# Optimization experiments

Measured on AMD Instinct MI355X. Metric: run time of the kernel, lower is better.

Reference implementation:

```python
import jax, jax.numpy as jnp
import numpy as np
import math

B, N, T, CI, CO = 4, 2048, 64, 32, 32
K, TAU = 6, 3


def _cheb(x, gso, k_order):
    # x: [b,n,t,c] complex, gso: [n,n] complex -> [K,b,n,t,c]
    polys = [x]
    if k_order > 1:
        polys.append(jnp.einsum('nm,bmtc->bntc', gso, x))
    for _ in range(2, k_order):
        polys.append(2.0 * jnp.einsum('nm,bmtc->bntc', gso, polys[-1]) - polys[-2])
    return jnp.stack(polys)


def _lag(p, tau):
    # shift along time axis (-2) by tau, zero-padding at the front
    if tau == 0:
        return p
    pad = jnp.zeros_like(p[..., :tau, :])
    return jnp.concatenate([pad, p[..., :-tau, :]], axis=-2)


def setup_inputs() -> dict:
    key = jax.random.key(0)
    ks = jax.random.split(key, 6)
    scale = 1.0 / math.sqrt(K * TAU * CI)
    gso_scale = 0.5 / math.sqrt(N)  # keep spectral radius ~<=1 for Cheb recursion
    return {
        'x_real': jax.random.normal(ks[0], (B, N, T, CI), jnp.float32),
        'x_imag': jax.random.normal(ks[1], (B, N, T, CI), jnp.float32),
        'gso_real': jax.random.normal(ks[2], (N, N), jnp.float32) * gso_scale,
        'gso_imag': jax.random.normal(ks[3], (N, N), jnp.float32) * gso_scale,
        'weight_real': jax.random.uniform(ks[4], (K, TAU, CI, CO), jnp.float32, -scale, scale),
        'weight_imag': jax.random.uniform(ks[5], (K, TAU, CI, CO), jnp.float32, -scale, scale),
        'bias_real': jnp.zeros((CO,), jnp.float32),
        'bias_imag': jnp.zeros((CO,), jnp.float32),
    }


def reference(x_real, x_imag, gso_real, gso_imag, weight_real, weight_imag, bias_real, bias_imag):
    x = jax.lax.complex(x_real, x_imag)
    gso = jax.lax.complex(gso_real, gso_imag)
    w = jax.lax.complex(weight_real, weight_imag)  # [K,TAU,i,o]
    bias = jax.lax.complex(bias_real, bias_imag)
    # Lag (time shift) and the graph shift act on different axes, so they
    # commute: compute the Chebyshev recursion ONCE on x, then lag the
    # stacked polynomials — same math as cheb(lag(x)) in the original.
    polys = _cheb(x, gso, K)  # [K,b,n,t,c]
    out = jnp.zeros((B, N, T, CO), dtype=polys.dtype)
    for tau in range(TAU):
        out = out + jnp.einsum('kbnti,kio->bnto', _lag(polys, tau), w[:, tau])
    return out + bias
```

## Files before the change

### kernel.cpp

```cpp
#include <hip/hip_runtime.h>
#include <stdint.h>

#define Bn 4
#define Nn 2048
#define Tn 64
#define CIn 32
#define COn 32
#define Kn 6
#define TAUn 3
#define Jn 8192

typedef _Float16 f16;
typedef _Float16 f16x2 __attribute__((ext_vector_type(2)));
typedef _Float16 f16x4 __attribute__((ext_vector_type(4)));
typedef _Float16 f16x8 __attribute__((ext_vector_type(8)));
typedef float f32x4 __attribute__((ext_vector_type(4)));

template <int N> struct ic { static constexpr int v = N; };

#if defined(__has_builtin)
#if __has_builtin(__builtin_amdgcn_fdot2)
#define HAVE_FDOT2 1
#endif
#endif

__device__ __forceinline__ float fdot2(f16x2 a, f16x2 b, float c) {
#ifdef HAVE_FDOT2
  return __builtin_amdgcn_fdot2(a, b, c, false);
#else
  return c + (float)a[0] * (float)b[0] + (float)a[1] * (float)b[1];
#endif
}

__device__ __forceinline__ void gld_lds16(const void* g, void* l) {
  auto gp = (const __attribute__((address_space(1))) uint32_t*)(uintptr_t)g;
  auto lp = (__attribute__((address_space(3))) uint32_t*)(uint32_t)(uintptr_t)l;
  __builtin_amdgcn_global_load_lds(gp, lp, 16, 0, 0);
}

__global__ __launch_bounds__(256) void pack_gso(const float* __restrict__ gr,
                                                const float* __restrict__ gi,
                                                f16* __restrict__ Gr,
                                                f16* __restrict__ Gi) {
  int u = blockIdx.x * 256 + threadIdx.x;
  float4 vr = ((const float4*)gr)[u];
  float4 vi = ((const float4*)gi)[u];
  f16x4 hr, hi;
  hr[0] = (f16)vr.x; hr[1] = (f16)vr.y; hr[2] = (f16)vr.z; hr[3] = (f16)vr.w;
  hi[0] = (f16)vi.x; hi[1] = (f16)vi.y; hi[2] = (f16)vi.z; hi[3] = (f16)vi.w;
  ((f16x4*)Gr)[u] = hr;
  ((f16x4*)Gi)[u] = hi;
}

__global__ __launch_bounds__(256) void pack_x(const float* __restrict__ xr,
                                              const float* __restrict__ xi,
                                              f16* __restrict__ P0) {
  __shared__ float tile[64][65];
  const int t = threadIdx.x;
  const int q0 = blockIdx.x * 64;
  const int n0 = blockIdx.y * 64;
  const int b = blockIdx.z;
  const int rr = t >> 4;
  const int cc = (t & 15) * 4;
  #pragma unroll
  for (int plane = 0; plane < 2; ++plane) {
    const float* src = plane ? xi : xr;
    if (plane) __syncthreads();
    #pragma unroll
    for (int it = 0; it < 4; ++it) {
      int n = it * 16 + rr;
      float4 v = *(const float4*)(src + ((size_t)b * Nn + n0 + n) * 2048 + q0 + cc);
      tile[n][cc + 0] = v.x; tile[n][cc + 1] = v.y;
      tile[n][cc + 2] = v.z; tile[n][cc + 3] = v.w;
    }
    __syncthreads();
    #pragma unroll
    for (int it = 0; it < 4; ++it) {
      int q = it * 16 + rr;
      f16x4 hv;
      hv[0] = (f16)tile[cc + 0][q];
      hv[1] = (f16)tile[cc + 1][q];
      hv[2] = (f16)tile[cc + 2][q];
      hv[3] = (f16)tile[cc + 3][q];
      *(f16x4*)(P0 + ((size_t)b * 2048 + q0 + q) * 4096 + plane * 2048 + n0 + cc) = hv;
    }
  }
}

__global__ __launch_bounds__(256) void pack_w(const float* __restrict__ wr,
                                              const float* __restrict__ wi,
                                              uint2* __restrict__ wpk) {
  int idx = blockIdx.x * 256 + threadIdx.x;
  if (idx >= Kn * TAUn * CIn * COn) return;
  float r = wr[idx], i = wi[idx];
  uint16_t hr = __builtin_bit_cast(uint16_t, (f16)r);
  uint16_t hi = __builtin_bit_cast(uint16_t, (f16)i);
  uint16_t hni = __builtin_bit_cast(uint16_t, (f16)(-i));
  uint2 o;
  o.x = (uint32_t)hr | ((uint32_t)hni << 16);
  o.y = (uint32_t)hi | ((uint32_t)hr << 16);
  wpk[idx] = o;
}

template <int MODE>
__global__ __launch_bounds__(256, 2) void cheb_gemm(
    const f16* __restrict__ Gr, const f16* __restrict__ Gi,
    const f16* __restrict__ P, f16* __restrict__ Q) {
  extern __shared__ __align__(16) char lds[];
  f16* L = (f16*)lds;

  const int tid = threadIdx.x;
  const int lane = tid & 63;
  const int w = tid >> 6;
  const int wm = w >> 1;
  const int wn = w & 1;
  const int sub = lane >> 4, rr = lane & 15;

  const int bid = blockIdx.x;
  const int xcd = bid & 7;
  const int l = bid >> 3;
  const int s = l & 63, wv = l >> 6;
  const int bj = xcd * 8 + (s >> 3);
  const int bn = (s & 7) + 8 * wv;
  const int n0 = bn * 128, j0 = bj * 128;
  const bool top = n0 < 2048;
  const int gmbase = n0 & 2047;

  const int trow = tid >> 3;
  const int cg = (tid & 7) ^ (trow & 7);
  const size_t aoffg = (size_t)(gmbase + trow) * 2048 + cg * 8;
  const size_t boffg = (size_t)(j0 + trow) * 4096 + cg * 8;
  const int sdst = w * 512;

  const int arb = rr * 64 + (sub ^ (rr & 3)) * 8;
  const int x32 = ((rr >> 2) & 1) * 32;
  const int kofs[2] = {x32, 32 - x32};

  auto stageA = [&](const f16* plane, int kcol, int h, int slot) {
    #pragma unroll
    for (int p = 0; p < 2; ++p)
      gld_lds16(plane + aoffg + h * 131072 + p * 65536 + kcol,
                L + slot * 4096 + sdst + p * 2048);
  };
  auto stageB = [&](int kt_, int h, int slot) {
    #pragma unroll
    for (int p = 0; p < 2; ++p)
      gld_lds16(P + boffg + h * 262144 + p * 131072 + kt_ * 64,
                L + slot * 4096 + sdst + p * 2048);
  };
  auto Aplane = [&](int kt_) -> const f16* {
    bool kr = (kt_ & 32) != 0;
    return top ? (kr ? Gi : Gr) : (kr ? Gr : Gi);
  };

  f32x4 acc[4][4] = {};
  f16x8 afr[2][2], bfr0[2][2], bfr1[2][2];

  stageB(0, 0, 2);
  stageA(Aplane(0), 0, 0, 0);
  stageA(Aplane(0), 0, 1, 1);
  stageB(0, 1, 3);
  stageB(1, 0, 6);
  stageA(Aplane(1), 64, 0, 4);

  for (int k2 = 0; k2 < 32; ++k2) {
    const int ktb = k2 * 2;

    auto tile = [&](auto ec) {
      constexpr int E = decltype(ec)::v;
      const int kt = ktb + E;
      const int ktn = (kt + 1) & 63;
      const int ktn2 = (kt + 2) & 63;
      const f16* apn = Aplane(ktn);
      const f16* apn2 = Aplane(ktn2);
      const int kcoln = (ktn * 64) & 2047;
      const int kcoln2 = (ktn2 * 64) & 2047;
      const bool negA = top && (kt & 32);

      auto loadA = [&](int qm) {
        #pragma unroll
        for (int f = 0; f < 2; ++f)
          #pragma unroll
          for (int ks = 0; ks < 2; ++ks)
            afr[f][ks] = *(const f16x8*)(
                L + (E * 4 + wm) * 4096 + qm * 2048 + f * 1024 + arb + kofs[ks]);
        if (negA) {
          #pragma unroll
          for (int f = 0; f < 2; ++f) { afr[f][0] = -afr[f][0]; afr[f][1] = -afr[f][1]; }
        }
      };
      auto loadB = [&](f16x8 (&bq)[2][2], int qn) {
        #pragma unroll
        for (int fc = 0; fc < 2; ++fc)
          #pragma unroll
          for (int ks = 0; ks < 2; ++ks)
            bq[fc][ks] = *(const f16x8*)(
                L + (E * 4 + 2 + wn) * 4096 + qn * 2048 + fc * 1024 + arb + kofs[ks]);
      };
      auto mf16 = [&](f16x8 (&bq)[2][2], int accR, int accC) {
        __builtin_amdgcn_s_setprio(1);
        #pragma unroll
        for (int ks = 0; ks < 2; ++ks)
          #pragma unroll
          for (int f = 0; f < 2; ++f)
            #pragma unroll
            for (int fc = 0; fc < 2; ++fc)
              acc[accR + f][accC + fc] = __builtin_amdgcn_mfma_f32_16x16x32_f16(
                  afr[f][ks], bq[fc][ks], acc[accR + f][accC + fc], 0, 0, 0);
        __builtin_amdgcn_s_setprio(0);
      };

      asm volatile("s_waitcnt vmcnt(4)" ::: "memory");
      __builtin_amdgcn_s_barrier();

      loadA(0); loadB(bfr0, 0);
      stageA(apn, kcoln, 1, (E ^ 1) * 4 + 1);
      mf16(bfr0, 0, 0);

      loadB(bfr1, 1);
      stageB(ktn, 1, (E ^ 1) * 4 + 3);
      mf16(bfr1, 0, 2);

      loadA(1);
      asm volatile("s_waitcnt lgkmcnt(0)" ::: "memory");
      __builtin_amdgcn_s_barrier();
      stageB(ktn2, 0, E * 4 + 2);
      mf16(bfr1, 2, 2);

      stageA(apn2, kcoln2, 0, E * 4 + 0);
      mf16(bfr0, 2, 0);
    };

    tile(ic<0>{});
    tile(ic<1>{});
  }

  asm volatile("s_waitcnt vmcnt(0)" ::: "memory");

  #pragma unroll
  for (int fc = 0; fc < 4; ++fc) {
    size_t j = (size_t)j0 + wn * 64 + fc * 16 + (lane & 15);
    #pragma unroll
    for (int fr = 0; fr < 4; ++fr) {
      int nn = n0 + wm * 64 + fr * 16 + ((lane >> 4) << 2);
      size_t off = j * 4096 + nn;
      f16x4 v;
      if (MODE == 1) {
        f16x4 o = *(const f16x4*)(Q + off);
        #pragma unroll
        for (int r = 0; r < 4; ++r)
          v[r] = (f16)(2.0f * acc[fr][fc][r] - (float)o[r]);
      } else {
        #pragma unroll
        for (int r = 0; r < 4; ++r)
          v[r] = (f16)acc[fr][fc][r];
      }
      *(f16x4*)(Q + off) = v;
    }
  }
}

template <bool CPLX>
__global__ __launch_bounds__(256, 3) void contract_k2(
    const f16* __restrict__ Pa, const f16* __restrict__ Pb,
    const uint2* __restrict__ wpk,
    const float* __restrict__ biasr, const float* __restrict__ biasi,
    float* __restrict__ out, int kbase) {
  __shared__ __align__(16) uint32_t Plds[128 * 64];
  __shared__ __align__(16) uint32_t WA[96 * 32];
  __shared__ __align__(16) uint32_t WB[CPLX ? 96 * 32 : 32];

  const int t = threadIdx.x;
  const int n0 = blockIdx.x * 64;
  const int t0 = blockIdx.y * 2;
  const int b = blockIdx.z;
  const int og = t & 7;
  const int ng = (t >> 3) & 15;
  const int tsl = t >> 7;

  float4 cur[4];
  if (!CPLX) {
    if (kbase == 0) {
      float4 bv = *(const float4*)(biasr + og * 4);
      #pragma unroll
      for (int nn = 0; nn < 4; ++nn) cur[nn] = bv;
    } else {
      const int tt = t0 + tsl;
      #pragma unroll
      for (int nn = 0; nn < 4; ++nn) {
        size_t n = (size_t)n0 + ng * 4 + nn;
        size_t ob = (((size_t)b * Nn + n) * Tn + tt) * COn + og * 4;
        cur[nn] = *(const float4*)(out + ob);
      }
    }
  }

  float aR[4][4] = {};
  float aI[4][4] = {};

  for (int h = 0; h < 2; ++h) {
    if (h) __syncthreads();
    const f16* Pc = h ? Pb : Pa;
    const int k = kbase + h;

    #pragma unroll
    for (int it = 0; it < 4; ++it) {
      int task = it * 256 + t;
      int row = task >> 3, oc = task & 7;
      int tp = (t0 - 2) * 32 + row;
      uint4 ur = {0, 0, 0, 0}, ui = {0, 0, 0, 0};
      if (tp >= 0) {
        size_t goff = ((size_t)b * 2048 + tp) * 4096 + n0 + oc * 8;
        ur = *(const uint4*)(Pc + goff);
        ui = *(const uint4*)(Pc + goff + 2048);
      }
      uint32_t* dst = &Plds[row * 64 + oc * 8];
      dst[0] = (ur.x & 0xffffu) | (ui.x << 16);
      dst[1] = (ur.x >> 16) | (ui.x & 0xffff0000u);
      dst[2] = (ur.y & 0xffffu) | (ui.y << 16);
      dst[3] = (ur.y >> 16) | (ui.y & 0xffff0000u);
      dst[4] = (ur.z & 0xffffu) | (ui.z << 16);
      dst[5] = (ur.z >> 16) | (ui.z & 0xffff0000u);
      dst[6] = (ur.w & 0xffffu) | (ui.w << 16);
      dst[7] = (ur.w >> 16) | (ui.w & 0xffff0000u);
    }
    #pragma unroll
    for (int it = 0; it < 12; ++it) {
      int idx = it * 256 + t;
      int q = idx >> 5, o = idx & 31;
      int tau = 2 - (q >> 5), ci = q & 31;
      uint2 wv = wpk[((k * TAUn + tau) * CIn + ci) * COn + o];
      WA[idx] = wv.x;
      if (CPLX) WB[idx] = wv.y;
    }
    __syncthreads();

    #pragma unroll 4
    for (int q = 0; q < 96; ++q) {
      uint4 wa = *(const uint4*)&WA[q * 32 + og * 4];
      const uint32_t* wap = &wa.x;
      uint4 wb;
      const uint32_t* wbp = &wb.x;
      if (CPLX) wb = *(const uint4*)&WB[q * 32 + og * 4];
      int row = tsl * 32 + q;
      uint4 pp = *(const uint4*)&Plds[row * 64 + ng * 4];
      const uint32_t* ppp = &pp.x;
      #pragma unroll
      for (int nn = 0; nn < 4; ++nn) {
        f16x2 hv = __builtin_bit_cast(f16x2, ppp[nn]);
        #pragma unroll
        for (int oo = 0; oo < 4; ++oo)
          aR[nn][oo] = fdot2(hv, __builtin_bit_cast(f16x2, wap[oo]), aR[nn][oo]);
        if (CPLX) {
          #pragma unroll
          for (int oo = 0; oo < 4; ++oo)
            aI[nn][oo] = fdot2(hv, __builtin_bit_cast(f16x2, wbp[oo]), aI[nn][oo]);
        }
      }
    }
  }

  const int tt = t0 + tsl;
  #pragma unroll
  for (int nn = 0; nn < 4; ++nn) {
    size_t n = (size_t)n0 + ng * 4 + nn;
    size_t ob = (((size_t)b * Nn + n) * Tn + tt) * COn + og * 4;
    if (!CPLX) {
      float4 v;
      v.x = aR[nn][0] + cur[nn].x;
      v.y = aR[nn][1] + cur[nn].y;
      v.z = aR[nn][2] + cur[nn].z;
      v.w = aR[nn][3] + cur[nn].w;
      *(float4*)(out + ob) = v;
    } else {
      float* po = out + ob * 2;
      float4 lo, hi;
      lo.x = aR[nn][0]; lo.y = aI[nn][0];
      lo.z = aR[nn][1]; lo.w = aI[nn][1];
      hi.x = aR[nn][2]; hi.y = aI[nn][2];
      hi.z = aR[nn][3]; hi.w = aI[nn][3];
      float4 c0, c1;
      if (kbase == 0) {
        const float* pr = biasr + og * 4;
        const float* pi = biasi + og * 4;
        c0 = make_float4(pr[0], pi[0], pr[1], pi[1]);
        c1 = make_float4(pr[2], pi[2], pr[3], pi[3]);
      } else {
        c0 = *(const float4*)(po);
        c1 = *(const float4*)(po + 4);
      }
      lo.x += c0.x; lo.y += c0.y; lo.z += c0.z; lo.w += c0.w;
      hi.x += c1.x; hi.y += c1.y; hi.z += c1.z; hi.w += c1.w;
      *(float4*)(po) = lo;
      *(float4*)(po + 4) = hi;
    }
  }
}

extern "C" void kernel_launch(void* const* d_in, const int* in_sizes, int n_in,
                              void* d_out, int out_size, void* d_ws, size_t ws_size,
                              hipStream_t stream) {
  (void)in_sizes; (void)n_in;
  const float* xr = (const float*)d_in[0];
  const float* xi = (const float*)d_in[1];
  const float* gr = (const float*)d_in[2];
  const float* gi = (const float*)d_in[3];
  const float* wr = (const float*)d_in[4];
  const float* wi = (const float*)d_in[5];
  const float* biasr = (const float*)d_in[6];
  const float* biasi = (const float*)d_in[7];
  float* out = (float*)d_out;

  const size_t PPLANE = (size_t)Jn * 4096 * sizeof(f16);
  const size_t GPLANE = (size_t)Nn * Nn * sizeof(f16);
  const size_t WPK = (size_t)Kn * TAUn * CIn * COn * 8;
  if (ws_size < 2 * PPLANE + 2 * GPLANE + WPK) return;

  char* ws = (char*)d_ws;
  f16* P0 = (f16*)(ws);
  f16* P1 = (f16*)(ws + PPLANE);
  f16* Gr = (f16*)(ws + 2 * PPLANE);
  f16* Gi = (f16*)(ws + 2 * PPLANE + GPLANE);
  uint2* wpk = (uint2*)(ws + 2 * PPLANE + 2 * GPLANE);

  const bool cplx = (out_size == 2 * Bn * Nn * Tn * COn);

  pack_gso<<<dim3(4096), dim3(256), 0, stream>>>(gr, gi, Gr, Gi);
  pack_x<<<dim3(32, 32, 4), dim3(256), 0, stream>>>(xr, xi, P0);
  pack_w<<<dim3(72), dim3(256), 0, stream>>>(wr, wi, wpk);

  #define CONTRACT2(KB, Pa, Pb)                                                    \
    do {                                                                           \
      if (cplx)                                                                    \
        contract_k2<true><<<dim3(32, 32, 4), dim3(256), 0, stream>>>(              \
            Pa, Pb, wpk, biasr, biasi, out, KB);                                   \
      else                                                                         \
        contract_k2<false><<<dim3(32, 32, 4), dim3(256), 0, stream>>>(             \
            Pa, Pb, wpk, biasr, biasi, out, KB);                                   \
    } while (0)

  cheb_gemm<0><<<dim3(2048), dim3(256), 65536, stream>>>(Gr, Gi, P0, P1);
  CONTRACT2(0, P0, P1);
  cheb_gemm<1><<<dim3(2048), dim3(256), 65536, stream>>>(Gr, Gi, P1, P0);
  cheb_gemm<1><<<dim3(2048), dim3(256), 65536, stream>>>(Gr, Gi, P0, P1);
  CONTRACT2(2, P0, P1);
  cheb_gemm<1><<<dim3(2048), dim3(256), 65536, stream>>>(Gr, Gi, P1, P0);
  cheb_gemm<1><<<dim3(2048), dim3(256), 65536, stream>>>(Gr, Gi, P0, P1);
  CONTRACT2(4, P0, P1);
  #undef CONTRACT2
}
```

Before: 1.853 ms.

## Use 3-multiply Gauss complex GEMM in Chebyshev recursion instead of 4-real embedding

The Chebyshev graph-shift GEMM previously embedded the complex product as a real GEMM over stacked real/imag planes, which amounts to four real products. It now computes three products per tile (Gr·Pr, Gi·Pi, (Gr+Gi)·(Pr+Pi)) into separate accumulators and forms the real and imaginary outputs in the epilogue, so each block writes both planes. Tiles are re-shaped to 128x64 with a 32-wide k step and the LDS footprint shrinks. The aim is to cut MFMA work by about a quarter. The cost is extra f16 vector adds and more accumulator registers, plus some precision risk from summing operands in f16.

```diff
diff --git a/kernel.cpp b/kernel.cpp
--- a/kernel.cpp
+++ b/kernel.cpp
@@ -103,7 +103,7 @@
 }
 
 template <int MODE>
-__global__ __launch_bounds__(256, 2) void cheb_gemm(
+__global__ __launch_bounds__(256, 2) void cheb_gemm3(
     const f16* __restrict__ Gr, const f16* __restrict__ Gi,
     const f16* __restrict__ P, f16* __restrict__ Q) {
   extern __shared__ __align__(16) char lds[];
@@ -119,116 +119,99 @@
   const int bid = blockIdx.x;
   const int xcd = bid & 7;
   const int l = bid >> 3;
-  const int s = l & 63, wv = l >> 6;
-  const int bj = xcd * 8 + (s >> 3);
-  const int bn = (s & 7) + 8 * wv;
-  const int n0 = bn * 128, j0 = bj * 128;
-  const bool top = n0 < 2048;
-  const int gmbase = n0 & 2047;
-
-  const int trow = tid >> 3;
-  const int cg = (tid & 7) ^ (trow & 7);
-  const size_t aoffg = (size_t)(gmbase + trow) * 2048 + cg * 8;
-  const size_t boffg = (size_t)(j0 + trow) * 4096 + cg * 8;
+  const int s = l & 63, w2 = l >> 6;
+  const int bj = xcd * 16 + (w2 & 1) * 8 + (s >> 3);
+  const int bn = (w2 >> 1) * 8 + (s & 7);
+  const int n0 = bn * 128, j0 = bj * 64;
+
+  const int srow = tid >> 2;
+  const int kcg = (tid & 3) ^ ((tid >> 3) & 3);
+  const size_t aoffg = (size_t)(n0 + srow) * 2048 + kcg * 8;
+  const size_t boffg = (size_t)(j0 + srow) * 4096 + kcg * 8;
   const int sdst = w * 512;
 
-  const int arb = rr * 64 + (sub ^ (rr & 3)) * 8;
-  const int x32 = ((rr >> 2) & 1) * 32;
-  const int kofs[2] = {x32, 32 - x32};
-
-  auto stageA = [&](const f16* plane, int kcol, int h, int slot) {
+  const int arb = rr * 32 + (sub ^ ((rr >> 1) & 3)) * 8;
+
+  auto stageA = [&](const f16* plane, int kcol, int slot) {
     #pragma unroll
     for (int p = 0; p < 2; ++p)
-      gld_lds16(plane + aoffg + h * 131072 + p * 65536 + kcol,
-                L + slot * 4096 + sdst + p * 2048);
+      gld_lds16(plane + aoffg + p * 131072 + kcol,
+                L + slot + p * 2048 + sdst);
   };
-  auto stageB = [&](int kt_, int h, int slot) {
-    #pragma unroll
-    for (int p = 0; p < 2; ++p)
-      gld_lds16(P + boffg + h * 262144 + p * 131072 + kt_ * 64,
-                L + slot * 4096 + sdst + p * 2048);
+  auto stageB = [&](int pl, int kcol, int slot) {
+    gld_lds16(P + boffg + pl * 2048 + kcol, L + slot + sdst);
   };
-  auto Aplane = [&](int kt_) -> const f16* {
-    bool kr = (kt_ & 32) != 0;
-    return top ? (kr ? Gi : Gr) : (kr ? Gr : Gi);
-  };
-
-  f32x4 acc[4][4] = {};
-  f16x8 afr[2][2], bfr0[2][2], bfr1[2][2];
-
-  stageB(0, 0, 2);
-  stageA(Aplane(0), 0, 0, 0);
-  stageA(Aplane(0), 0, 1, 1);
-  stageB(0, 1, 3);
-  stageB(1, 0, 6);
-  stageA(Aplane(1), 64, 0, 4);
+
+  f32x4 ac1[4][2] = {}, ac2[4][2] = {}, ac3[4][2] = {};
+  f16x8 ar[4], ai[4], br[2], bi[2];
+
+  stageA(Gr, 0, 0);
+  stageA(Gi, 0, 4096);
+  stageB(0, 0, 8192);
+  stageB(1, 0, 10240);
+  stageA(Gr, 32, 12288);
+  stageA(Gi, 32, 16384);
+  stageB(0, 32, 20480);
+  stageB(1, 32, 22528);
 
   for (int k2 = 0; k2 < 32; ++k2) {
     const int ktb = k2 * 2;
 
     auto tile = [&](auto ec) {
       constexpr int E = decltype(ec)::v;
+      constexpr int AB = E * 12288;
       const int kt = ktb + E;
-      const int ktn = (kt + 1) & 63;
-      const int ktn2 = (kt + 2) & 63;
-      const f16* apn = Aplane(ktn);
-      const f16* apn2 = Aplane(ktn2);
-      const int kcoln = (ktn * 64) & 2047;
-      const int kcoln2 = (ktn2 * 64) & 2047;
-      const bool negA = top && (kt & 32);
-
-      auto loadA = [&](int qm) {
-        #pragma unroll
-        for (int f = 0; f < 2; ++f)
-          #pragma unroll
-          for (int ks = 0; ks < 2; ++ks)
-            afr[f][ks] = *(const f16x8*)(
-                L + (E * 4 + wm) * 4096 + qm * 2048 + f * 1024 + arb + kofs[ks]);
-        if (negA) {
-          #pragma unroll
-          for (int f = 0; f < 2; ++f) { afr[f][0] = -afr[f][0]; afr[f][1] = -afr[f][1]; }
-        }
-      };
-      auto loadB = [&](f16x8 (&bq)[2][2], int qn) {
-        #pragma unroll
-        for (int fc = 0; fc < 2; ++fc)
-          #pragma unroll
-          for (int ks = 0; ks < 2; ++ks)
-            bq[fc][ks] = *(const f16x8*)(
-                L + (E * 4 + 2 + wn) * 4096 + qn * 2048 + fc * 1024 + arb + kofs[ks]);
-      };
-      auto mf16 = [&](f16x8 (&bq)[2][2], int accR, int accC) {
-        __builtin_amdgcn_s_setprio(1);
-        #pragma unroll
-        for (int ks = 0; ks < 2; ++ks)
-          #pragma unroll
-          for (int f = 0; f < 2; ++f)
-            #pragma unroll
-            for (int fc = 0; fc < 2; ++fc)
-              acc[accR + f][accC + fc] = __builtin_amdgcn_mfma_f32_16x16x32_f16(
-                  afr[f][ks], bq[fc][ks], acc[accR + f][accC + fc], 0, 0, 0);
-        __builtin_amdgcn_s_setprio(0);
-      };
-
-      asm volatile("s_waitcnt vmcnt(4)" ::: "memory");
+      const int kcol2 = ((kt + 2) & 63) * 32;
+
+      asm volatile("s_waitcnt vmcnt(6)" ::: "memory");
       __builtin_amdgcn_s_barrier();
 
-      loadA(0); loadB(bfr0, 0);
-      stageA(apn, kcoln, 1, (E ^ 1) * 4 + 1);
-      mf16(bfr0, 0, 0);
-
-      loadB(bfr1, 1);
-      stageB(ktn, 1, (E ^ 1) * 4 + 3);
-      mf16(bfr1, 0, 2);
-
-      loadA(1);
+      #pragma unroll
+      for (int f = 0; f < 4; ++f) {
+        int ro = wm * 2048 + f * 512 + arb;
+        ar[f] = *(const f16x8*)(L + AB + ro);
+        ai[f] = *(const f16x8*)(L + AB + 4096 + ro);
+      }
+      #pragma unroll
+      for (int fc = 0; fc < 2; ++fc) {
+        int ro = wn * 1024 + fc * 512 + arb;
+        br[fc] = *(const f16x8*)(L + AB + 8192 + ro);
+        bi[fc] = *(const f16x8*)(L + AB + 10240 + ro);
+      }
+
       asm volatile("s_waitcnt lgkmcnt(0)" ::: "memory");
       __builtin_amdgcn_s_barrier();
-      stageB(ktn2, 0, E * 4 + 2);
-      mf16(bfr1, 2, 2);
-
-      stageA(apn2, kcoln2, 0, E * 4 + 0);
-      mf16(bfr0, 2, 0);
+      stageA(Gr, kcol2, AB);
+      stageA(Gi, kcol2, AB + 4096);
+      stageB(0, kcol2, AB + 8192);
+      stageB(1, kcol2, AB + 10240);
+
+      __builtin_amdgcn_s_setprio(1);
+      #pragma unroll
+      for (int f = 0; f < 4; ++f)
+        #pragma unroll
+        for (int fc = 0; fc < 2; ++fc)
+          ac1[f][fc] = __builtin_amdgcn_mfma_f32_16x16x32_f16(
+              ar[f], br[fc], ac1[f][fc], 0, 0, 0);
+      #pragma unroll
+      for (int f = 0; f < 4; ++f)
+        #pragma unroll
+        for (int fc = 0; fc < 2; ++fc)
+          ac2[f][fc] = __builtin_amdgcn_mfma_f32_16x16x32_f16(
+              ai[f], bi[fc], ac2[f][fc], 0, 0, 0);
+      __builtin_amdgcn_s_setprio(0);
+      #pragma unroll
+      for (int f = 0; f < 4; ++f) ar[f] = ar[f] + ai[f];
+      #pragma unroll
+      for (int fc = 0; fc < 2; ++fc) br[fc] = br[fc] + bi[fc];
+      __builtin_amdgcn_s_setprio(1);
+      #pragma unroll
+      for (int f = 0; f < 4; ++f)
+        #pragma unroll
+        for (int fc = 0; fc < 2; ++fc)
+          ac3[f][fc] = __builtin_amdgcn_mfma_f32_16x16x32_f16(
+              ar[f], br[fc], ac3[f][fc], 0, 0, 0);
+      __builtin_amdgcn_s_setprio(0);
     };
 
     tile(ic<0>{});
@@ -238,24 +221,32 @@
   asm volatile("s_waitcnt vmcnt(0)" ::: "memory");
 
   #pragma unroll
-  for (int fc = 0; fc < 4; ++fc) {
-    size_t j = (size_t)j0 + wn * 64 + fc * 16 + (lane & 15);
+  for (int fc = 0; fc < 2; ++fc) {
+    size_t j = (size_t)j0 + wn * 32 + fc * 16 + (lane & 15);
     #pragma unroll
     for (int fr = 0; fr < 4; ++fr) {
       int nn = n0 + wm * 64 + fr * 16 + ((lane >> 4) << 2);
-      size_t off = j * 4096 + nn;
-      f16x4 v;
+      size_t offr = j * 4096 + nn;
+      f16x4 vr, vi;
       if (MODE == 1) {
-        f16x4 o = *(const f16x4*)(Q + off);
-        #pragma unroll
-        for (int r = 0; r < 4; ++r)
-          v[r] = (f16)(2.0f * acc[fr][fc][r] - (float)o[r]);
+        f16x4 qr = *(const f16x4*)(Q + offr);
+        f16x4 qi = *(const f16x4*)(Q + offr + 2048);
+        #pragma unroll
+        for (int r = 0; r < 4; ++r) {
+          float m1 = ac1[fr][fc][r], m2 = ac2[fr][fc][r], m3 = ac3[fr][fc][r];
+          vr[r] = (f16)(2.0f * (m1 - m2) - (float)qr[r]);
+          vi[r] = (f16)(2.0f * (m3 - m1 - m2) - (float)qi[r]);
+        }
       } else {
         #pragma unroll
-        for (int r = 0; r < 4; ++r)
-          v[r] = (f16)acc[fr][fc][r];
-      }
-      *(f16x4*)(Q + off) = v;
+        for (int r = 0; r < 4; ++r) {
+          float m1 = ac1[fr][fc][r], m2 = ac2[fr][fc][r], m3 = ac3[fr][fc][r];
+          vr[r] = (f16)(m1 - m2);
+          vi[r] = (f16)(m3 - m1 - m2);
+        }
+      }
+      *(f16x4*)(Q + offr) = vr;
+      *(f16x4*)(Q + offr + 2048) = vi;
     }
   }
 }
@@ -439,13 +430,13 @@
             Pa, Pb, wpk, biasr, biasi, out, KB);                                   \
     } while (0)
 
-  cheb_gemm<0><<<dim3(2048), dim3(256), 65536, stream>>>(Gr, Gi, P0, P1);
+  cheb_gemm3<0><<<dim3(2048), dim3(256), 49152, stream>>>(Gr, Gi, P0, P1);
   CONTRACT2(0, P0, P1);
-  cheb_gemm<1><<<dim3(2048), dim3(256), 65536, stream>>>(Gr, Gi, P1, P0);
-  cheb_gemm<1><<<dim3(2048), dim3(256), 65536, stream>>>(Gr, Gi, P0, P1);
+  cheb_gemm3<1><<<dim3(2048), dim3(256), 49152, stream>>>(Gr, Gi, P1, P0);
+  cheb_gemm3<1><<<dim3(2048), dim3(256), 49152, stream>>>(Gr, Gi, P0, P1);
   CONTRACT2(2, P0, P1);
-  cheb_gemm<1><<<dim3(2048), dim3(256), 65536, stream>>>(Gr, Gi, P1, P0);
-  cheb_gemm<1><<<dim3(2048), dim3(256), 65536, stream>>>(Gr, Gi, P0, P1);
+  cheb_gemm3<1><<<dim3(2048), dim3(256), 49152, stream>>>(Gr, Gi, P1, P0);
+  cheb_gemm3<1><<<dim3(2048), dim3(256), 49152, stream>>>(Gr, Gi, P0, P1);
   CONTRACT2(4, P0, P1);
   #undef CONTRACT2
 }
```

Result: faster. 1.812 ms (-2.2%).
